# Kernel tuning notes

Measured on AMD Instinct MI355X. Metric: run time of the kernel, lower is better.

The kernel has to match this reference:

```python
import jax, jax.numpy as jnp
import numpy as np

B, S, E, H = 2, 2048, 1024, 16
D = E // H  # head_dim = 64


def setup_inputs() -> dict:
    key = jax.random.key(0)
    ks = jax.random.split(key, 5)
    return {
        "hidden_states": jax.random.normal(ks[0], (B, S, E), jnp.float32),
        "c_attn_w": jax.random.normal(ks[1], (E, 3 * E), jnp.float32) * 0.02,
        "c_attn_b": jax.random.normal(ks[2], (3 * E,), jnp.float32) * 0.02,
        "c_proj_w": jax.random.normal(ks[3], (E, E), jnp.float32) * 0.02,
        "c_proj_b": jax.random.normal(ks[4], (E,), jnp.float32) * 0.02,
    }


def reference(hidden_states, c_attn_w, c_attn_b, c_proj_w, c_proj_b):
    # Conv1D: y = x @ W + b, W is [in, out]
    qkv = hidden_states @ c_attn_w + c_attn_b            # [B,S,3E]
    q, k, v = jnp.split(qkv, 3, axis=-1)                 # each [B,S,E]

    def split_heads(t):
        return t.reshape(B, S, H, D).transpose(0, 2, 1, 3)  # [B,H,S,D]

    q, k, v = split_heads(q), split_heads(k), split_heads(v)

    # scores scaled by 1/sqrt(head_dim) (scale_attn_weights=True)
    scores = jnp.einsum("bhqd,bhkd->bhqk", q, k) / jnp.asarray(
        np.sqrt(D), dtype=q.dtype
    )
    # causal mask: torch.where(causal, scores, finfo.min)
    causal = jnp.tril(jnp.ones((S, S), dtype=bool))
    mask_value = jnp.finfo(scores.dtype).min
    scores = jnp.where(causal[None, None], scores, mask_value)

    attn = jax.nn.softmax(scores, axis=-1)               # [B,H,S,S]
    out = jnp.einsum("bhqk,bhkd->bhqd", attn, v)          # [B,H,S,D]
    out = out.transpose(0, 2, 1, 3).reshape(B, S, E)      # merge heads
    out = out @ c_proj_w + c_proj_b                       # c_proj
    return out
```

## Files before the change

### kernel.cpp

```cpp
#include <hip/hip_runtime.h>
#include <stdint.h>

#define LOG2E 1.4426950408889634f
#define QSCALE (0.125f * LOG2E)

using u16 = unsigned short;
using u32 = unsigned int;

typedef __attribute__((ext_vector_type(8))) short short8;
typedef __attribute__((ext_vector_type(4))) float f32x4;
typedef __attribute__((ext_vector_type(16))) float f32x16;

__device__ __forceinline__ u16 f32_bf16(float f) {
  union { float f; u32 u; } v; v.f = f;
  u32 u = v.u;
  u += 0x7FFF + ((u >> 16) & 1);
  return (u16)(u >> 16);
}

__device__ __forceinline__ float max3f(float a, float b, float c) {
  return fmaxf(fmaxf(a, b), c);
}

__device__ __forceinline__ void gload_lds16(const void* g, void* l) {
  __builtin_amdgcn_global_load_lds(
      (const __attribute__((address_space(1))) u32*)(uintptr_t)g,
      (__attribute__((address_space(3))) u32*)(u32)(uintptr_t)l, 16, 0, 0);
}


__global__ __launch_bounds__(256) void cvt_f32_bf16(const float* __restrict__ in,
                                                    u16* __restrict__ out, int n4) {
  for (int i = blockIdx.x * blockDim.x + threadIdx.x; i < n4;
       i += gridDim.x * blockDim.x) {
    float4 v = ((const float4*)in)[i];
    union { u16 h[4]; uint2 u; } o;
    o.h[0] = f32_bf16(v.x); o.h[1] = f32_bf16(v.y);
    o.h[2] = f32_bf16(v.z); o.h[3] = f32_bf16(v.w);
    ((uint2*)out)[i] = o.u;
  }
}

__global__ __launch_bounds__(256) void transpose_bf16(const float* __restrict__ in,
                                                      u16* __restrict__ out,
                                                      int K, int N) {
  __shared__ float t[32][33];
  const int n0 = blockIdx.x * 32, k0 = blockIdx.y * 32;
  const int tx = threadIdx.x, ty = threadIdx.y;
#pragma unroll
  for (int j = 0; j < 32; j += 8)
    t[ty + j][tx] = in[(size_t)(k0 + ty + j) * N + n0 + tx];
  __syncthreads();
#pragma unroll
  for (int j = 0; j < 32; j += 8)
    out[(size_t)(n0 + ty + j) * K + k0 + tx] = f32_bf16(t[tx][ty + j]);
}

template <int MODE>
__global__ __launch_bounds__(256) void gemm_bt(
    const u16* __restrict__ A, const u16* __restrict__ Bt,
    const float* __restrict__ bias,
    u16* __restrict__ qb, u16* __restrict__ kb, u16* __restrict__ vtb,
    float* __restrict__ fout) {
  __shared__ u16 lA[128 * 32];
  __shared__ u16 lB[128 * 32];
  const int tid = threadIdx.x;
  const int w = tid >> 6, l = tid & 63;
  const int bm = blockIdx.y, bn = blockIdx.x;
  const size_t m0 = (size_t)bm * 128, n0 = (size_t)bn * 128;
  const int wr = w >> 1, wc = w & 1;

  f32x4 acc[4][4] = {};

  const int arow = w * 16 + (l >> 2);
  const int acol = (l & 3) * 8;
  const u16* gA = A + (m0 + arow) * 1024 + acol;
  const u16* gB = Bt + (n0 + arow) * 1024 + acol;
  u16* lAw = lA + w * 512;
  u16* lBw = lB + w * 512;

  for (int k0 = 0; k0 < 1024; k0 += 32) {
    gload_lds16(gA + k0, lAw);
    gload_lds16(gA + k0 + 64 * 1024, lAw + 2048);
    gload_lds16(gB + k0, lBw);
    gload_lds16(gB + k0 + 64 * 1024, lBw + 2048);
    __syncthreads();
    short8 af[4], bf[4];
#pragma unroll
    for (int m = 0; m < 4; ++m)
      af[m] = *(const short8*)&lA[(wr * 64 + m * 16 + (l & 15)) * 32 + (l >> 4) * 8];
#pragma unroll
    for (int n = 0; n < 4; ++n)
      bf[n] = *(const short8*)&lB[(wc * 64 + n * 16 + (l & 15)) * 32 + (l >> 4) * 8];
#pragma unroll
    for (int m = 0; m < 4; ++m)
#pragma unroll
      for (int n = 0; n < 4; ++n)
        acc[m][n] = __builtin_amdgcn_mfma_f32_16x16x32_bf16(af[m], bf[n], acc[m][n], 0, 0, 0);
    __syncthreads();
  }

  if (MODE == 0) {
#pragma unroll
    for (int m = 0; m < 4; ++m) {
      const int row = (int)m0 + wr * 64 + m * 16 + ((l >> 4) << 2);
      const int b = row >> 11, s = row & 2047;
#pragma unroll
      for (int n = 0; n < 4; ++n) {
        const int col = (int)n0 + wc * 64 + n * 16 + (l & 15);
        const int part = col >> 10;
        const int h = (col & 1023) >> 6, d = col & 63;
        const float bv = bias[col];
        const size_t bh = (size_t)(b * 16 + h);
#pragma unroll
        for (int r = 0; r < 4; ++r) {
          const float v = acc[m][n][r] + bv;
          const int ss = s + r;
          if (part == 0)
            qb[(bh * 2048 + ss) * 64 + d] = f32_bf16(v * QSCALE);
          else if (part == 1)
            kb[(bh * 2048 + ss) * 64 + d] = f32_bf16(v);
          else
            vtb[(bh * 64 + d) * 2048 + ss] = f32_bf16(v);
        }
      }
    }
  } else {
#pragma unroll
    for (int m = 0; m < 4; ++m) {
      const size_t row = m0 + wr * 64 + m * 16 + ((l >> 4) << 2);
#pragma unroll
      for (int n = 0; n < 4; ++n) {
        const size_t col = n0 + wc * 64 + n * 16 + (l & 15);
        const float bv = bias[col];
#pragma unroll
        for (int r = 0; r < 4; ++r)
          fout[(row + r) * 1024 + col] = acc[m][n][r] + bv;
      }
    }
  }
}

__global__ __launch_bounds__(256) void attn_fwd6(const u16* __restrict__ Qb,
                                                 const u16* __restrict__ Kb,
                                                 const u16* __restrict__ Vt,
                                                 u16* __restrict__ AO) {
  __shared__ u16 lK[2][4096];
  __shared__ u16 lV[2][4096];
  const int tid = threadIdx.x;
  const int l = tid & 63, w = tid >> 6;
  const int lq = l & 31, hi = l >> 5;
  const int bid = blockIdx.x;
  const int xcd = bid & 7, idx = bid >> 3;
  const int bh = xcd * 4 + (idx & 3);
  const int qb = 15 - (idx >> 2);
  const int qw = qb * 128 + w * 32;
  const int q = qw + lq;
  const int cdiag = 2 * qb + (w >> 1);
  const int NT = 2 * qb + 2;

  const u16* Qh = Qb + (size_t)bh * 131072;
  const u16* Kh = Kb + (size_t)bh * 131072;
  const u16* Vh = Vt + (size_t)bh * 131072;

  short8 qf[4];
#pragma unroll
  for (int kk = 0; kk < 4; ++kk)
    qf[kk] = *(const short8*)&Qh[(size_t)q * 64 + kk * 16 + hi * 8];

  f32x16 oA = {}, oB = {};
  float m = -3.0e38f, lsum = 0.f;

  const int srow = l >> 3, sslot = l & 7;
  const int swz = ((sslot ^ srow) << 3);
  const u16* kbase = Kh + (16 * w + srow) * 64 + swz;
  const u16* vbase = Vh + (size_t)(16 * w + srow) * 2048 + swz;
  char* lKw0 = (char*)&lK[0][0] + 2 * w * 1024;
  char* lVw0 = (char*)&lV[0][0] + 2 * w * 1024;

  auto stage = [&](int buf, int c) {
    const u16* ks = kbase + c * 4096;
    const u16* vs = vbase + c * 64;
    char* kd = lKw0 + buf * 8192;
    char* vd = lVw0 + buf * 8192;
    gload_lds16(ks, kd);
    gload_lds16(ks + 512, kd + 1024);
    gload_lds16(vs, vd);
    gload_lds16(vs + 16384, vd + 1024);
  };

  const int swsl = (lq & 7);

  auto pack16 = [&](const f32x16& st, short8& lo, short8& hi8) {
    u32 pk[8];
#pragma unroll
    for (int t2 = 0; t2 < 8; ++t2)
      asm("v_cvt_pk_bf16_f32 %0, %1, %2" : "=v"(pk[t2]) : "v"(st[2 * t2]), "v"(st[2 * t2 + 1]));
    u32 a0 = pk[0], a1 = pk[2]; asm("v_permlane32_swap_b32 %0, %1" : "+v"(a0), "+v"(a1));
    u32 a2 = pk[1], a3 = pk[3]; asm("v_permlane32_swap_b32 %0, %1" : "+v"(a2), "+v"(a3));
    u32 c0 = pk[4], c1 = pk[6]; asm("v_permlane32_swap_b32 %0, %1" : "+v"(c0), "+v"(c1));
    u32 c2 = pk[5], c3 = pk[7]; asm("v_permlane32_swap_b32 %0, %1" : "+v"(c2), "+v"(c3));
    union { u32 u[4]; short8 s; } f0, f1;
    f0.u[0] = a0; f0.u[1] = a2; f0.u[2] = a1; f0.u[3] = a3;
    f1.u[0] = c0; f1.u[1] = c2; f1.u[2] = c1; f1.u[3] = c3;
    lo = f0.s; hi8 = f1.s;
  };

  auto body64 = [&](int buf, bool mask2) {
    const char* kb = (const char*)&lK[buf][0] + lq * 128;
    const char* vb = (const char*)&lV[buf][0] + lq * 128;
    short8 kf0[4], kf1[4];
#pragma unroll
    for (int kk = 0; kk < 4; ++kk) {
      const int sl = ((2 * kk + hi) ^ swsl) << 4;
      kf0[kk] = *(const short8*)(kb + sl);
      kf1[kk] = *(const short8*)(kb + 4096 + sl);
    }
    f32x16 st0 = {}, st1 = {};
    __builtin_amdgcn_s_setprio(1);
#pragma unroll
    for (int kk = 0; kk < 4; ++kk)
      st0 = __builtin_amdgcn_mfma_f32_32x32x16_bf16(kf0[kk], qf[kk], st0, 0, 0, 0);
#pragma unroll
    for (int kk = 0; kk < 4; ++kk)
      st1 = __builtin_amdgcn_mfma_f32_32x32x16_bf16(kf1[kk], qf[kk], st1, 0, 0, 0);
    __builtin_amdgcn_s_setprio(0);

    short8 vfA[4], vfB[4];
#pragma unroll
    for (int ks = 0; ks < 4; ++ks) {
      const int sl = ((2 * ks + hi) ^ swsl) << 4;
      vfA[ks] = *(const short8*)(vb + sl);
      vfB[ks] = *(const short8*)(vb + 4096 + sl);
    }

    if (mask2) {
      const int qm = lq - hi * 4;
#pragma unroll
      for (int r = 0; r < 16; ++r) {
        const int t = (r & 3) + 8 * (r >> 2);
        if (t > qm) st1[r] = -3.0e38f;
      }
    }

    float a0 = max3f(st0[0], st0[1], st0[2]);
    float a1 = max3f(st0[3], st0[4], st0[5]);
    float a2 = max3f(st0[6], st0[7], st0[8]);
    float a3 = max3f(st0[9], st0[10], st0[11]);
    float a4 = max3f(st0[12], st0[13], st0[14]);
    float a5 = max3f(st0[15], st1[0], st1[1]);
    float a6 = max3f(st1[2], st1[3], st1[4]);
    float a7 = max3f(st1[5], st1[6], st1[7]);
    float a8 = max3f(st1[8], st1[9], st1[10]);
    float a9 = max3f(st1[11], st1[12], st1[13]);
    float a10 = fmaxf(st1[14], st1[15]);
    float b0 = max3f(a0, a1, a2);
    float b1 = max3f(a3, a4, a5);
    float b2 = max3f(a6, a7, a8);
    float b3 = max3f(a9, a10, b0);
    float pm = max3f(b1, b2, b3);
    pm = fmaxf(pm, __shfl_xor(pm, 32));

    if (!__all(pm <= m + 8.0f)) {
      const float mn = fmaxf(m, pm);
      const float alpha = __builtin_amdgcn_exp2f(m - mn);
      lsum *= alpha;
#pragma unroll
      for (int r = 0; r < 16; ++r) { oA[r] *= alpha; oB[r] *= alpha; }
      m = mn;
    }

#pragma unroll
    for (int r = 0; r < 16; ++r) st0[r] = __builtin_amdgcn_exp2f(st0[r] - m);
#pragma unroll
    for (int r = 0; r < 16; ++r) st1[r] = __builtin_amdgcn_exp2f(st1[r] - m);

    float s0 = (st0[0] + st0[1]) + (st0[2] + st0[3]);
    float s1 = (st0[4] + st0[5]) + (st0[6] + st0[7]);
    float s2 = (st0[8] + st0[9]) + (st0[10] + st0[11]);
    float s3 = (st0[12] + st0[13]) + (st0[14] + st0[15]);
    float s4 = (st1[0] + st1[1]) + (st1[2] + st1[3]);
    float s5 = (st1[4] + st1[5]) + (st1[6] + st1[7]);
    float s6 = (st1[8] + st1[9]) + (st1[10] + st1[11]);
    float s7 = (st1[12] + st1[13]) + (st1[14] + st1[15]);
    float rs = ((s0 + s1) + (s2 + s3)) + ((s4 + s5) + (s6 + s7));
    rs += __shfl_xor(rs, 32);
    lsum += rs;

    short8 pf0, pf1, pf2, pf3;
    pack16(st0, pf0, pf1);
    pack16(st1, pf2, pf3);

    __builtin_amdgcn_s_setprio(1);
    oA = __builtin_amdgcn_mfma_f32_32x32x16_bf16(vfA[0], pf0, oA, 0, 0, 0);
    oA = __builtin_amdgcn_mfma_f32_32x32x16_bf16(vfA[1], pf1, oA, 0, 0, 0);
    oA = __builtin_amdgcn_mfma_f32_32x32x16_bf16(vfA[2], pf2, oA, 0, 0, 0);
    oA = __builtin_amdgcn_mfma_f32_32x32x16_bf16(vfA[3], pf3, oA, 0, 0, 0);
    oB = __builtin_amdgcn_mfma_f32_32x32x16_bf16(vfB[0], pf0, oB, 0, 0, 0);
    oB = __builtin_amdgcn_mfma_f32_32x32x16_bf16(vfB[1], pf1, oB, 0, 0, 0);
    oB = __builtin_amdgcn_mfma_f32_32x32x16_bf16(vfB[2], pf2, oB, 0, 0, 0);
    oB = __builtin_amdgcn_mfma_f32_32x32x16_bf16(vfB[3], pf3, oB, 0, 0, 0);
    __builtin_amdgcn_s_setprio(0);
  };

  auto body32m = [&](int buf) {
    const char* kb = (const char*)&lK[buf][0] + lq * 128;
    const char* vb = (const char*)&lV[buf][0] + lq * 128;
    short8 kf0[4];
#pragma unroll
    for (int kk = 0; kk < 4; ++kk)
      kf0[kk] = *(const short8*)(kb + (((2 * kk + hi) ^ swsl) << 4));
    f32x16 st0 = {};
    __builtin_amdgcn_s_setprio(1);
#pragma unroll
    for (int kk = 0; kk < 4; ++kk)
      st0 = __builtin_amdgcn_mfma_f32_32x32x16_bf16(kf0[kk], qf[kk], st0, 0, 0, 0);
    __builtin_amdgcn_s_setprio(0);

    short8 vfA[2], vfB[2];
#pragma unroll
    for (int ks = 0; ks < 2; ++ks) {
      const int sl = ((2 * ks + hi) ^ swsl) << 4;
      vfA[ks] = *(const short8*)(vb + sl);
      vfB[ks] = *(const short8*)(vb + 4096 + sl);
    }

    const int qm = lq - hi * 4;
#pragma unroll
    for (int r = 0; r < 16; ++r) {
      const int t = (r & 3) + 8 * (r >> 2);
      if (t > qm) st0[r] = -3.0e38f;
    }
    float a0 = max3f(st0[0], st0[1], st0[2]);
    float a1 = max3f(st0[3], st0[4], st0[5]);
    float a2 = max3f(st0[6], st0[7], st0[8]);
    float a3 = max3f(st0[9], st0[10], st0[11]);
    float a4 = max3f(st0[12], st0[13], st0[14]);
    float b0 = max3f(a0, a1, a2);
    float b1 = max3f(a3, a4, st0[15]);
    float pm = fmaxf(b0, b1);
    pm = fmaxf(pm, __shfl_xor(pm, 32));
    if (!__all(pm <= m + 8.0f)) {
      const float mn = fmaxf(m, pm);
      const float alpha = __builtin_amdgcn_exp2f(m - mn);
      lsum *= alpha;
#pragma unroll
      for (int r = 0; r < 16; ++r) { oA[r] *= alpha; oB[r] *= alpha; }
      m = mn;
    }
#pragma unroll
    for (int r = 0; r < 16; ++r) st0[r] = __builtin_amdgcn_exp2f(st0[r] - m);
    float s0 = (st0[0] + st0[1]) + (st0[2] + st0[3]);
    float s1 = (st0[4] + st0[5]) + (st0[6] + st0[7]);
    float s2 = (st0[8] + st0[9]) + (st0[10] + st0[11]);
    float s3 = (st0[12] + st0[13]) + (st0[14] + st0[15]);
    float rs = (s0 + s1) + (s2 + s3);
    rs += __shfl_xor(rs, 32);
    lsum += rs;

    short8 pf0, pf1;
    pack16(st0, pf0, pf1);
    __builtin_amdgcn_s_setprio(1);
    oA = __builtin_amdgcn_mfma_f32_32x32x16_bf16(vfA[0], pf0, oA, 0, 0, 0);
    oA = __builtin_amdgcn_mfma_f32_32x32x16_bf16(vfA[1], pf1, oA, 0, 0, 0);
    oB = __builtin_amdgcn_mfma_f32_32x32x16_bf16(vfB[0], pf0, oB, 0, 0, 0);
    oB = __builtin_amdgcn_mfma_f32_32x32x16_bf16(vfB[1], pf1, oB, 0, 0, 0);
    __builtin_amdgcn_s_setprio(0);
  };

  stage(0, 0);
  __syncthreads();
  int cur = 0;
  for (int c = 0; c < NT; ++c) {
    if (c + 1 < NT) stage(cur ^ 1, c + 1);
    if (c < cdiag) body64(cur, false);
    else if (c == cdiag) { if (w & 1) body64(cur, true); else body32m(cur); }
    __syncthreads();
    cur ^= 1;
  }

  const float rl = __builtin_amdgcn_rcpf(lsum);
  const int b = bh >> 4, h = bh & 15;
  u16* orow = AO + ((size_t)(b * 2048 + q)) * 1024 + h * 64;
#pragma unroll
  for (int g = 0; g < 4; ++g) {
    float e0 = oA[4 * g] * rl, e1 = oA[4 * g + 1] * rl;
    float e2 = oA[4 * g + 2] * rl, e3 = oA[4 * g + 3] * rl;
    float f0 = oB[4 * g] * rl, f1 = oB[4 * g + 1] * rl;
    float f2 = oB[4 * g + 2] * rl, f3 = oB[4 * g + 3] * rl;
    u32 w0, w1, w2, w3;
    asm("v_cvt_pk_bf16_f32 %0, %1, %2" : "=v"(w0) : "v"(e0), "v"(e1));
    asm("v_cvt_pk_bf16_f32 %0, %1, %2" : "=v"(w1) : "v"(e2), "v"(e3));
    asm("v_cvt_pk_bf16_f32 %0, %1, %2" : "=v"(w2) : "v"(f0), "v"(f1));
    asm("v_cvt_pk_bf16_f32 %0, %1, %2" : "=v"(w3) : "v"(f2), "v"(f3));
    uint2 uA; uA.x = w0; uA.y = w1;
    uint2 uB; uB.x = w2; uB.y = w3;
    *(uint2*)&orow[8 * g + 4 * hi] = uA;
    *(uint2*)&orow[32 + 8 * g + 4 * hi] = uB;
  }
}


extern "C" void kernel_launch(void* const* d_in, const int* in_sizes, int n_in,
                              void* d_out, int out_size, void* d_ws, size_t ws_size,
                              hipStream_t stream) {
  const float* hs = (const float*)d_in[0];
  const float* w1 = (const float*)d_in[1];
  const float* b1 = (const float*)d_in[2];
  const float* w2 = (const float*)d_in[3];
  const float* b2 = (const float*)d_in[4];
  float* out = (float*)d_out;

  char* ws = (char*)d_ws;
  u16* Xb  = (u16*)(ws);
  u16* W1t = (u16*)(ws + (8ull  << 20));
  u16* W2t = (u16*)(ws + (14ull << 20));
  u16* Qb  = (u16*)(ws + (16ull << 20));
  u16* Kb  = (u16*)(ws + (24ull << 20));
  u16* Vtb = (u16*)(ws + (32ull << 20));
  u16* AO  = (u16*)(ws + (40ull << 20));

  cvt_f32_bf16<<<dim3(2048), dim3(256), 0, stream>>>(hs, Xb, 4096 * 1024 / 4);
  transpose_bf16<<<dim3(96, 32), dim3(32, 8), 0, stream>>>(w1, W1t, 1024, 3072);
  transpose_bf16<<<dim3(32, 32), dim3(32, 8), 0, stream>>>(w2, W2t, 1024, 1024);
  gemm_bt<0><<<dim3(24, 32), dim3(256), 0, stream>>>(Xb, W1t, b1, Qb, Kb, Vtb, nullptr);
  attn_fwd6<<<dim3(512), dim3(256), 0, stream>>>(Qb, Kb, Vtb, AO);
  gemm_bt<1><<<dim3(8, 32), dim3(256), 0, stream>>>(AO, W2t, b2, nullptr, nullptr, nullptr, out);
}
```

Baseline: 125.1 us.

## Rewrite QKV GEMM with 256x256 tiles, 4-stage LDS pipeline and swizzle

Replaces the QKV projection GEMM with a 512-thread kernel that computes 256x256 output tiles. It uses a 4-slot LDS ring buffer with three tiles prefetched ahead, XOR-swizzled LDS addressing to avoid bank conflicts, and MFMA phases raised in priority with setprio. For the V columns the MFMA operands are swapped, so the transposed V output is written with contiguous sequence indices. The goal is to hide global load latency behind compute and to improve data reuse and store coalescing, at the cost of 128KB of LDS per block and a grid of only 192 blocks.

```diff
diff --git a/kernel.cpp b/kernel.cpp
--- a/kernel.cpp
+++ b/kernel.cpp
@@ -56,12 +56,158 @@
     out[(size_t)(n0 + ty + j) * K + k0 + tx] = f32_bf16(t[tx][ty + j]);
 }
 
-template <int MODE>
-__global__ __launch_bounds__(256) void gemm_bt(
+__global__ __launch_bounds__(512) void gemm_qkv8(
     const u16* __restrict__ A, const u16* __restrict__ Bt,
     const float* __restrict__ bias,
-    u16* __restrict__ qb, u16* __restrict__ kb, u16* __restrict__ vtb,
-    float* __restrict__ fout) {
+    u16* __restrict__ qb, u16* __restrict__ kb, u16* __restrict__ vtb) {
+  __shared__ u16 lds[65536];
+  const int tid = threadIdx.x;
+  const int l = tid & 63, w = tid >> 6;
+  const int l15 = l & 15, l4 = l >> 4;
+  const int wm = w >> 2, wn = w & 3;
+  const int bm = blockIdx.y, bn = blockIdx.x;
+  const size_t m0 = (size_t)bm * 256;
+  const int nb = bn * 256;
+  const bool sw = bn >= 8;
+
+  const u16* gsrc[4];
+#pragma unroll
+  for (int q = 0; q < 4; ++q) {
+    const int c = (w * 4 + q) * 64 + l;
+    const int mat = c >> 10;
+    const int pc = c & 1023;
+    const int pair = pc >> 3, s8 = pc & 7;
+    const int us8 = s8 ^ (pair & 7);
+    const int grow = pair * 2 + (us8 >> 2);
+    const int kslot = us8 & 3;
+    gsrc[q] = (mat == 0 ? A + (m0 + grow) * 1024
+                        : Bt + (size_t)(nb + grow) * 1024) + kslot * 8;
+  }
+
+  auto stage2 = [&](int slot, int t, int qbase) {
+#pragma unroll
+    for (int q = 0; q < 2; ++q)
+      gload_lds16(gsrc[qbase + q] + t * 32,
+                  &lds[slot * 16384 + (w * 4 + qbase + q) * 512]);
+  };
+
+  auto rdA = [&](int slot, int mI) -> short8 {
+    const int row = wm * 128 + mI * 16 + l15;
+    const int pair = row >> 1;
+    const int s8 = (((row & 1) << 2) + l4) ^ (pair & 7);
+    return *(const short8*)&lds[slot * 16384 + pair * 64 + s8 * 8];
+  };
+  auto rdB = [&](int slot, int nI) -> short8 {
+    const int row = wn * 64 + nI * 16 + l15;
+    const int pair = row >> 1;
+    const int s8 = (((row & 1) << 2) + l4) ^ (pair & 7);
+    return *(const short8*)&lds[slot * 16384 + 8192 + pair * 64 + s8 * 8];
+  };
+
+  f32x4 acc[8][4] = {};
+
+  auto mfma16 = [&](const short8* af4, const short8* bf4, int mbase) {
+    if (!sw) {
+#pragma unroll
+      for (int n = 0; n < 4; ++n)
+#pragma unroll
+        for (int mm = 0; mm < 4; ++mm)
+          acc[mbase + mm][n] = __builtin_amdgcn_mfma_f32_16x16x32_bf16(
+              af4[mm], bf4[n], acc[mbase + mm][n], 0, 0, 0);
+    } else {
+#pragma unroll
+      for (int n = 0; n < 4; ++n)
+#pragma unroll
+        for (int mm = 0; mm < 4; ++mm)
+          acc[mbase + mm][n] = __builtin_amdgcn_mfma_f32_16x16x32_bf16(
+              bf4[n], af4[mm], acc[mbase + mm][n], 0, 0, 0);
+    }
+  };
+
+#pragma unroll
+  for (int tt = 0; tt < 3; ++tt) {
+    stage2(tt, tt, 0);
+    stage2(tt, tt, 2);
+  }
+  asm volatile("s_waitcnt vmcnt(0)" ::: "memory");
+  __builtin_amdgcn_s_barrier();
+
+  for (int t = 0; t < 32; ++t) {
+    const int slot = t & 3;
+    const int sst = (t + 3) & 3;
+    const bool st = t <= 28;
+    short8 bfr[4], afr[4];
+#pragma unroll
+    for (int n = 0; n < 4; ++n) bfr[n] = rdB(slot, n);
+#pragma unroll
+    for (int mm = 0; mm < 4; ++mm) afr[mm] = rdA(slot, mm);
+    if (st) stage2(sst, t + 3, 0);
+    __builtin_amdgcn_s_barrier();
+    asm volatile("s_waitcnt lgkmcnt(0)" ::: "memory");
+    __builtin_amdgcn_sched_barrier(0);
+    __builtin_amdgcn_s_setprio(1);
+    mfma16(afr, bfr, 0);
+    __builtin_amdgcn_s_setprio(0);
+    __builtin_amdgcn_s_barrier();
+#pragma unroll
+    for (int mm = 0; mm < 4; ++mm) afr[mm] = rdA(slot, 4 + mm);
+    if (st) stage2(sst, t + 3, 2);
+    __builtin_amdgcn_s_barrier();
+    asm volatile("s_waitcnt lgkmcnt(0)" ::: "memory");
+    __builtin_amdgcn_sched_barrier(0);
+    __builtin_amdgcn_s_setprio(1);
+    mfma16(afr, bfr, 4);
+    __builtin_amdgcn_s_setprio(0);
+    if (t <= 28)      asm volatile("s_waitcnt vmcnt(8)" ::: "memory");
+    else if (t == 29) asm volatile("s_waitcnt vmcnt(4)" ::: "memory");
+    else if (t == 30) asm volatile("s_waitcnt vmcnt(0)" ::: "memory");
+    __builtin_amdgcn_s_barrier();
+  }
+
+  if (!sw) {
+#pragma unroll
+    for (int mm = 0; mm < 8; ++mm) {
+      const int row = (int)m0 + wm * 128 + mm * 16 + (l4 << 2);
+      const int b = row >> 11, s = row & 2047;
+#pragma unroll
+      for (int n = 0; n < 4; ++n) {
+        const int col = nb + wn * 64 + n * 16 + l15;
+        const int part = col >> 10;
+        const int h = (col & 1023) >> 6, d = col & 63;
+        const float bv = bias[col];
+        const size_t bh = (size_t)(b * 16 + h);
+        u16* dst = (part == 0) ? qb : kb;
+        const float sc = (part == 0) ? QSCALE : 1.0f;
+#pragma unroll
+        for (int r = 0; r < 4; ++r)
+          dst[(bh * 2048 + (s + r)) * 64 + d] = f32_bf16((acc[mm][n][r] + bv) * sc);
+      }
+    }
+  } else {
+#pragma unroll
+    for (int mm = 0; mm < 8; ++mm) {
+      const int scol = (int)m0 + wm * 128 + mm * 16 + l15;
+      const int b = scol >> 11, s = scol & 2047;
+#pragma unroll
+      for (int n = 0; n < 4; ++n) {
+        const int colg = nb + wn * 64 + n * 16 + (l4 << 2);
+        const float4 bv4 = *(const float4*)&bias[colg];
+        const float bvr[4] = { bv4.x, bv4.y, bv4.z, bv4.w };
+#pragma unroll
+        for (int r = 0; r < 4; ++r) {
+          const int dcol = colg + r - 2048;
+          const int h = dcol >> 6, d = dcol & 63;
+          const size_t bh = (size_t)(b * 16 + h);
+          vtb[bh * 131072 + (size_t)d * 2048 + s] = f32_bf16(acc[mm][n][r] + bvr[r]);
+        }
+      }
+    }
+  }
+}
+
+__global__ __launch_bounds__(256) void gemm_proj(
+    const u16* __restrict__ A, const u16* __restrict__ Bt,
+    const float* __restrict__ bias, float* __restrict__ fout) {
   __shared__ u16 lA[128 * 32];
   __shared__ u16 lB[128 * 32];
   const int tid = threadIdx.x;
@@ -100,43 +246,16 @@
     __syncthreads();
   }
 
-  if (MODE == 0) {
-#pragma unroll
-    for (int m = 0; m < 4; ++m) {
-      const int row = (int)m0 + wr * 64 + m * 16 + ((l >> 4) << 2);
-      const int b = row >> 11, s = row & 2047;
-#pragma unroll
-      for (int n = 0; n < 4; ++n) {
-        const int col = (int)n0 + wc * 64 + n * 16 + (l & 15);
-        const int part = col >> 10;
-        const int h = (col & 1023) >> 6, d = col & 63;
-        const float bv = bias[col];
-        const size_t bh = (size_t)(b * 16 + h);
-#pragma unroll
-        for (int r = 0; r < 4; ++r) {
-          const float v = acc[m][n][r] + bv;
-          const int ss = s + r;
-          if (part == 0)
-            qb[(bh * 2048 + ss) * 64 + d] = f32_bf16(v * QSCALE);
-          else if (part == 1)
-            kb[(bh * 2048 + ss) * 64 + d] = f32_bf16(v);
-          else
-            vtb[(bh * 64 + d) * 2048 + ss] = f32_bf16(v);
-        }
-      }
-    }
-  } else {
-#pragma unroll
-    for (int m = 0; m < 4; ++m) {
-      const size_t row = m0 + wr * 64 + m * 16 + ((l >> 4) << 2);
-#pragma unroll
-      for (int n = 0; n < 4; ++n) {
-        const size_t col = n0 + wc * 64 + n * 16 + (l & 15);
-        const float bv = bias[col];
-#pragma unroll
-        for (int r = 0; r < 4; ++r)
-          fout[(row + r) * 1024 + col] = acc[m][n][r] + bv;
-      }
+#pragma unroll
+  for (int m = 0; m < 4; ++m) {
+    const size_t row = m0 + wr * 64 + m * 16 + ((l >> 4) << 2);
+#pragma unroll
+    for (int n = 0; n < 4; ++n) {
+      const size_t col = n0 + wc * 64 + n * 16 + (l & 15);
+      const float bv = bias[col];
+#pragma unroll
+      for (int r = 0; r < 4; ++r)
+        fout[(row + r) * 1024 + col] = acc[m][n][r] + bv;
     }
   }
 }
@@ -423,7 +542,7 @@
   cvt_f32_bf16<<<dim3(2048), dim3(256), 0, stream>>>(hs, Xb, 4096 * 1024 / 4);
   transpose_bf16<<<dim3(96, 32), dim3(32, 8), 0, stream>>>(w1, W1t, 1024, 3072);
   transpose_bf16<<<dim3(32, 32), dim3(32, 8), 0, stream>>>(w2, W2t, 1024, 1024);
-  gemm_bt<0><<<dim3(24, 32), dim3(256), 0, stream>>>(Xb, W1t, b1, Qb, Kb, Vtb, nullptr);
+  gemm_qkv8<<<dim3(12, 16), dim3(512), 0, stream>>>(Xb, W1t, b1, Qb, Kb, Vtb);
   attn_fwd6<<<dim3(512), dim3(256), 0, stream>>>(Qb, Kb, Vtb, AO);
-  gemm_bt<1><<<dim3(8, 32), dim3(256), 0, stream>>>(AO, W2t, b2, nullptr, nullptr, nullptr, out);
-}
+  gemm_proj<<<dim3(8, 32), dim3(256), 0, stream>>>(AO, W2t, b2, out);
+}
```

New measurement: 129.6 us. 1.04x slower.

## Swizzle GEMM LDS layout and split attention into 64-query two-wave blocks

Applied to the files above, without the earlier changes.

The GEMM now stores A/B tiles in LDS as row pairs with an XOR swizzle, so the MFMA fragment reads avoid bank conflicts. The attention kernel changes from 256-thread blocks over 128 queries to 128-thread blocks over 64 queries with 1024 blocks. Each wave now stages more K/V rows, which gives finer causal load balancing and more blocks per CU. The cost is less K/V reuse per staged tile and more blocks to schedule.

```diff
diff --git a/kernel.cpp b/kernel.cpp
--- a/kernel.cpp
+++ b/kernel.cpp
@@ -57,25 +57,29 @@
 }
 
 template <int MODE>
-__global__ __launch_bounds__(256) void gemm_bt(
+__global__ __launch_bounds__(256) void gemm_bt3(
     const u16* __restrict__ A, const u16* __restrict__ Bt,
     const float* __restrict__ bias,
     u16* __restrict__ qb, u16* __restrict__ kb, u16* __restrict__ vtb,
     float* __restrict__ fout) {
-  __shared__ u16 lA[128 * 32];
-  __shared__ u16 lB[128 * 32];
+  __shared__ u16 lA[4096];
+  __shared__ u16 lB[4096];
   const int tid = threadIdx.x;
   const int w = tid >> 6, l = tid & 63;
+  const int l15 = l & 15, l4 = l >> 4;
+  const int wr = w >> 1, wc = w & 1;
   const int bm = blockIdx.y, bn = blockIdx.x;
   const size_t m0 = (size_t)bm * 128, n0 = (size_t)bn * 128;
-  const int wr = w >> 1, wc = w & 1;
 
   f32x4 acc[4][4] = {};
 
-  const int arow = w * 16 + (l >> 2);
-  const int acol = (l & 3) * 8;
-  const u16* gA = A + (m0 + arow) * 1024 + acol;
-  const u16* gB = Bt + (n0 + arow) * 1024 + acol;
+  const int c = w * 64 + l;
+  const int pair0 = c >> 3, s80 = c & 7;
+  const int us8 = s80 ^ (pair0 & 7);
+  const int grow = 2 * pair0 + (us8 >> 2);
+  const int kslot = us8 & 3;
+  const u16* gA = A + (m0 + grow) * 1024 + kslot * 8;
+  const u16* gB = Bt + (n0 + grow) * 1024 + kslot * 8;
   u16* lAw = lA + w * 512;
   u16* lBw = lB + w * 512;
 
@@ -87,34 +91,42 @@
     __syncthreads();
     short8 af[4], bf[4];
 #pragma unroll
-    for (int m = 0; m < 4; ++m)
-      af[m] = *(const short8*)&lA[(wr * 64 + m * 16 + (l & 15)) * 32 + (l >> 4) * 8];
-#pragma unroll
-    for (int n = 0; n < 4; ++n)
-      bf[n] = *(const short8*)&lB[(wc * 64 + n * 16 + (l & 15)) * 32 + (l >> 4) * 8];
-#pragma unroll
-    for (int m = 0; m < 4; ++m)
+    for (int mI = 0; mI < 4; ++mI) {
+      const int row = wr * 64 + mI * 16 + l15;
+      const int pr = row >> 1;
+      const int s8 = (((row & 1) << 2) | l4) ^ (pr & 7);
+      af[mI] = *(const short8*)((const char*)lA + pr * 128 + s8 * 16);
+    }
+#pragma unroll
+    for (int n = 0; n < 4; ++n) {
+      const int row = wc * 64 + n * 16 + l15;
+      const int pr = row >> 1;
+      const int s8 = (((row & 1) << 2) | l4) ^ (pr & 7);
+      bf[n] = *(const short8*)((const char*)lB + pr * 128 + s8 * 16);
+    }
+#pragma unroll
+    for (int mI = 0; mI < 4; ++mI)
 #pragma unroll
       for (int n = 0; n < 4; ++n)
-        acc[m][n] = __builtin_amdgcn_mfma_f32_16x16x32_bf16(af[m], bf[n], acc[m][n], 0, 0, 0);
+        acc[mI][n] = __builtin_amdgcn_mfma_f32_16x16x32_bf16(af[mI], bf[n], acc[mI][n], 0, 0, 0);
     __syncthreads();
   }
 
   if (MODE == 0) {
 #pragma unroll
-    for (int m = 0; m < 4; ++m) {
-      const int row = (int)m0 + wr * 64 + m * 16 + ((l >> 4) << 2);
+    for (int mI = 0; mI < 4; ++mI) {
+      const int row = (int)m0 + wr * 64 + mI * 16 + (l4 << 2);
       const int b = row >> 11, s = row & 2047;
 #pragma unroll
       for (int n = 0; n < 4; ++n) {
-        const int col = (int)n0 + wc * 64 + n * 16 + (l & 15);
+        const int col = (int)n0 + wc * 64 + n * 16 + l15;
         const int part = col >> 10;
         const int h = (col & 1023) >> 6, d = col & 63;
         const float bv = bias[col];
         const size_t bh = (size_t)(b * 16 + h);
 #pragma unroll
         for (int r = 0; r < 4; ++r) {
-          const float v = acc[m][n][r] + bv;
+          const float v = acc[mI][n][r] + bv;
           const int ss = s + r;
           if (part == 0)
             qb[(bh * 2048 + ss) * 64 + d] = f32_bf16(v * QSCALE);
@@ -127,21 +139,21 @@
     }
   } else {
 #pragma unroll
-    for (int m = 0; m < 4; ++m) {
-      const size_t row = m0 + wr * 64 + m * 16 + ((l >> 4) << 2);
+    for (int mI = 0; mI < 4; ++mI) {
+      const size_t row = m0 + wr * 64 + mI * 16 + (l4 << 2);
 #pragma unroll
       for (int n = 0; n < 4; ++n) {
-        const size_t col = n0 + wc * 64 + n * 16 + (l & 15);
+        const size_t col = n0 + wc * 64 + n * 16 + l15;
         const float bv = bias[col];
 #pragma unroll
         for (int r = 0; r < 4; ++r)
-          fout[(row + r) * 1024 + col] = acc[m][n][r] + bv;
+          fout[(row + r) * 1024 + col] = acc[mI][n][r] + bv;
       }
     }
   }
 }
 
-__global__ __launch_bounds__(256) void attn_fwd6(const u16* __restrict__ Qb,
+__global__ __launch_bounds__(128) void attn_fwd7(const u16* __restrict__ Qb,
                                                  const u16* __restrict__ Kb,
                                                  const u16* __restrict__ Vt,
                                                  u16* __restrict__ AO) {
@@ -153,11 +165,9 @@
   const int bid = blockIdx.x;
   const int xcd = bid & 7, idx = bid >> 3;
   const int bh = xcd * 4 + (idx & 3);
-  const int qb = 15 - (idx >> 2);
-  const int qw = qb * 128 + w * 32;
-  const int q = qw + lq;
-  const int cdiag = 2 * qb + (w >> 1);
-  const int NT = 2 * qb + 2;
+  const int qb = 31 - (idx >> 2);
+  const int q = qb * 64 + w * 32 + lq;
+  const int NT = qb + 1;
 
   const u16* Qh = Qb + (size_t)bh * 131072;
   const u16* Kh = Kb + (size_t)bh * 131072;
@@ -173,20 +183,19 @@
 
   const int srow = l >> 3, sslot = l & 7;
   const int swz = ((sslot ^ srow) << 3);
-  const u16* kbase = Kh + (16 * w + srow) * 64 + swz;
-  const u16* vbase = Vh + (size_t)(16 * w + srow) * 2048 + swz;
-  char* lKw0 = (char*)&lK[0][0] + 2 * w * 1024;
-  char* lVw0 = (char*)&lV[0][0] + 2 * w * 1024;
+  const u16* kbase = Kh + (32 * w + srow) * 64 + swz;
+  const u16* vbase = Vh + (size_t)(32 * w + srow) * 2048 + swz;
 
   auto stage = [&](int buf, int c) {
     const u16* ks = kbase + c * 4096;
     const u16* vs = vbase + c * 64;
-    char* kd = lKw0 + buf * 8192;
-    char* vd = lVw0 + buf * 8192;
-    gload_lds16(ks, kd);
-    gload_lds16(ks + 512, kd + 1024);
-    gload_lds16(vs, vd);
-    gload_lds16(vs + 16384, vd + 1024);
+    char* kd = (char*)&lK[buf][0] + w * 4096;
+    char* vd = (char*)&lV[buf][0] + w * 4096;
+#pragma unroll
+    for (int i = 0; i < 4; ++i) {
+      gload_lds16(ks + 512 * i, kd + 1024 * i);
+      gload_lds16(vs + 16384 * i, vd + 1024 * i);
+    }
   };
 
   const int swsl = (lq & 7);
@@ -373,8 +382,8 @@
   int cur = 0;
   for (int c = 0; c < NT; ++c) {
     if (c + 1 < NT) stage(cur ^ 1, c + 1);
-    if (c < cdiag) body64(cur, false);
-    else if (c == cdiag) { if (w & 1) body64(cur, true); else body32m(cur); }
+    if (c < qb) body64(cur, false);
+    else { if (w) body64(cur, true); else body32m(cur); }
     __syncthreads();
     cur ^= 1;
   }
@@ -423,7 +432,7 @@
   cvt_f32_bf16<<<dim3(2048), dim3(256), 0, stream>>>(hs, Xb, 4096 * 1024 / 4);
   transpose_bf16<<<dim3(96, 32), dim3(32, 8), 0, stream>>>(w1, W1t, 1024, 3072);
   transpose_bf16<<<dim3(32, 32), dim3(32, 8), 0, stream>>>(w2, W2t, 1024, 1024);
-  gemm_bt<0><<<dim3(24, 32), dim3(256), 0, stream>>>(Xb, W1t, b1, Qb, Kb, Vtb, nullptr);
-  attn_fwd6<<<dim3(512), dim3(256), 0, stream>>>(Qb, Kb, Vtb, AO);
-  gemm_bt<1><<<dim3(8, 32), dim3(256), 0, stream>>>(AO, W2t, b2, nullptr, nullptr, nullptr, out);
-}
+  gemm_bt3<0><<<dim3(24, 32), dim3(256), 0, stream>>>(Xb, W1t, b1, Qb, Kb, Vtb, nullptr);
+  attn_fwd7<<<dim3(1024), dim3(128), 0, stream>>>(Qb, Kb, Vtb, AO);
+  gemm_bt3<1><<<dim3(8, 32), dim3(256), 0, stream>>>(AO, W2t, b2, nullptr, nullptr, nullptr, out);
+}
```

Measured after the change: 126.6 us. About the same (+1.1%).
